# Optimization experiments

Measured on AMD Instinct MI355X. Metric: run time of the kernel, lower is better.

Reference implementation:

```python
import jax, jax.numpy as jnp
import numpy as np

D_MODEL = 1024
NUM_HEADS = 16
HEAD_DIM = D_MODEL // NUM_HEADS
B, S = 4, 2048


def setup_inputs() -> dict:
    key = jax.random.key(0)
    ks = jax.random.split(key, 11)
    scale = 1.0 / np.sqrt(D_MODEL)
    return {
        "query": jax.random.normal(ks[0], (B, S, D_MODEL), dtype=jnp.float32),
        "key": jax.random.normal(ks[1], (B, S, D_MODEL), dtype=jnp.float32),
        "value": jax.random.normal(ks[2], (B, S, D_MODEL), dtype=jnp.float32),
        "Wq": jax.random.normal(ks[3], (D_MODEL, D_MODEL), dtype=jnp.float32) * scale,
        "bq": jnp.zeros((D_MODEL,), dtype=jnp.float32),
        "Wk": jax.random.normal(ks[4], (D_MODEL, D_MODEL), dtype=jnp.float32) * scale,
        "bk": jnp.zeros((D_MODEL,), dtype=jnp.float32),
        "Wv": jax.random.normal(ks[5], (D_MODEL, D_MODEL), dtype=jnp.float32) * scale,
        "bv": jnp.zeros((D_MODEL,), dtype=jnp.float32),
        "Wo": jax.random.normal(ks[6], (D_MODEL, D_MODEL), dtype=jnp.float32) * scale,
        "bo": jnp.zeros((D_MODEL,), dtype=jnp.float32),
    }


def reference(query, key, value, Wq, bq, Wk, bk, Wv, bv, Wo, bo):
    b = query.shape[0]
    # QKV projections, split into heads: [B, H, S, hd]
    Q = (query @ Wq + bq).reshape(b, -1, NUM_HEADS, HEAD_DIM).transpose(0, 2, 1, 3)
    K = (key @ Wk + bk).reshape(b, -1, NUM_HEADS, HEAD_DIM).transpose(0, 2, 1, 3)
    V = (value @ Wv + bv).reshape(b, -1, NUM_HEADS, HEAD_DIM).transpose(0, 2, 1, 3)
    # scaled dot-product attention, full [B, H, S, S] scores (as in original)
    scores = jnp.einsum("bhqd,bhkd->bhqk", Q, K) / jnp.sqrt(
        jnp.asarray(HEAD_DIM, dtype=jnp.float32))
    attn = jax.nn.softmax(scores, axis=-1)
    out = jnp.einsum("bhqk,bhkd->bhqd", attn, V)
    out = out.transpose(0, 2, 1, 3).reshape(b, -1, D_MODEL)
    return out @ Wo + bo
```

## Files before the change

### kernel.cpp

```cpp
#include <hip/hip_runtime.h>
#include <hip/hip_bf16.h>

typedef _Float16 f16;
typedef _Float16 f16x8 __attribute__((ext_vector_type(8)));
typedef _Float16 f16x4 __attribute__((ext_vector_type(4)));
typedef __fp16 h16x2 __attribute__((ext_vector_type(2)));
typedef float f32x4 __attribute__((ext_vector_type(4)));

#define D_MODEL 1024
#define NHEAD 16
#define HD 64
#define BATCH 4
#define SEQ 2048
#define TOK (BATCH * SEQ)

__device__ __forceinline__ void gload_lds16(const void* g, void* l) {
  __builtin_amdgcn_global_load_lds(
      (const __attribute__((address_space(1))) unsigned int*)g,
      (__attribute__((address_space(3))) unsigned int*)l, 16, 0, 0);
}

__device__ __forceinline__ f16x8 fragF16_64(const char* rowptr, int g, int c) {
  union { uint4 u; f16x8 v; } r;
  r.u = *reinterpret_cast<const uint4*>(rowptr + ((g * 16) ^ ((c & 3) << 4)));
  return r.v;
}
__device__ __forceinline__ f16x8 fragF32_128(const char* rowptr, int g, int c) {
  const int s = (c & 7) << 4;
  union { uint4 u; float f[4]; } a, b;
  a.u = *reinterpret_cast<const uint4*>(rowptr + ((g * 32) ^ s));
  b.u = *reinterpret_cast<const uint4*>(rowptr + ((g * 32 + 16) ^ s));
  f16x8 r;
  r[0] = (f16)a.f[0]; r[1] = (f16)a.f[1]; r[2] = (f16)a.f[2]; r[3] = (f16)a.f[3];
  r[4] = (f16)b.f[0]; r[5] = (f16)b.f[1]; r[6] = (f16)b.f[2]; r[7] = (f16)b.f[3];
  return r;
}
__device__ __forceinline__ f16x8 lds_frag(const char* rowptr, int cb0, int s) {
  const uint2 a = *reinterpret_cast<const uint2*>(rowptr + (cb0 ^ s));
  const uint2 b = *reinterpret_cast<const uint2*>(rowptr + ((cb0 + 32) ^ s));
  union { unsigned int u[4]; f16x8 v; } r;
  r.u[0] = a.x; r.u[1] = a.y; r.u[2] = b.x; r.u[3] = b.y;
  return r.v;
}

__global__ __launch_bounds__(256) void transpose_cvt4_k(
    const float* __restrict__ w0, const float* __restrict__ w1,
    const float* __restrict__ w2, const float* __restrict__ w3,
    f16* __restrict__ t0, f16* __restrict__ t1, f16* __restrict__ t2,
    f16* __restrict__ t3) {
  __shared__ float tile[32][33];
  const float* W = blockIdx.z == 0 ? w0 : blockIdx.z == 1 ? w1 : blockIdx.z == 2 ? w2 : w3;
  f16* Wt = blockIdx.z == 0 ? t0 : blockIdx.z == 1 ? t1 : blockIdx.z == 2 ? t2 : t3;
  int n0 = blockIdx.x * 32, k0 = blockIdx.y * 32;
  int tx = threadIdx.x & 31, ty = threadIdx.x >> 5;
#pragma unroll
  for (int i = 0; i < 32; i += 8)
    tile[ty + i][tx] = W[(size_t)(k0 + ty + i) * D_MODEL + n0 + tx];
  __syncthreads();
#pragma unroll
  for (int i = 0; i < 32; i += 8)
    Wt[(size_t)(n0 + ty + i) * D_MODEL + k0 + tx] = (f16)tile[tx][ty + i];
}

__device__ __forceinline__ void swz_map(int& btx, int& bty) {
  int lin = blockIdx.x + blockIdx.y * 8;
  int xcd = lin & 7, rest = lin >> 3;
  bty = xcd * 8 + (rest & 7);
  btx = rest >> 3;
}

template <bool A_F32, bool B_F32, bool OUT_F32, bool BIAS_ROW>
__device__ __forceinline__ void gemm_body(
    const void* __restrict__ Ap, const void* __restrict__ Bp,
    const float* __restrict__ bias, void* __restrict__ Cout,
    int M, int N, int K, float scale, int btx, int bty) {
  constexpr int ABUF = A_F32 ? 16384 : 8192;
  constexpr int BBUF = B_F32 ? 16384 : 8192;
  constexpr int BUF = ABUF + BBUF;
  constexpr int NA = A_F32 ? 4 : 2;
  constexpr int NB = B_F32 ? 4 : 2;
  __shared__ char smem[2 * BUF];
  const int tid = threadIdx.x;
  const int lane = tid & 63, wid = tid >> 6;
  const int g = lane >> 4, c = lane & 15;
  const int wm = wid >> 1, wn = wid & 1;
  const size_t brow = (size_t)bty * 128, bcol = (size_t)btx * 128;

  f32x4 acc[4][4];
#pragma unroll
  for (int i = 0; i < 4; ++i)
#pragma unroll
    for (int j = 0; j < 4; ++j) acc[i][j] = (f32x4){0.f, 0.f, 0.f, 0.f};

  const char* ga[NA];
  const char* gb[NB];
#pragma unroll
  for (int j = 0; j < NA; ++j) {
    int ch = wid * NA + j;
    if constexpr (A_F32) {
      int row = ch * 8 + (lane >> 3);
      ga[j] = (const char*)Ap + ((size_t)(brow + row) * K) * 4 +
              (((lane & 7) * 16) ^ ((row & 7) << 4));
    } else {
      int row = ch * 16 + (lane >> 2);
      ga[j] = (const char*)Ap + ((size_t)(brow + row) * K) * 2 +
              (((lane & 3) * 16) ^ ((row & 3) << 4));
    }
  }
#pragma unroll
  for (int j = 0; j < NB; ++j) {
    int ch = wid * NB + j;
    if constexpr (B_F32) {
      int row = ch * 8 + (lane >> 3);
      gb[j] = (const char*)Bp + ((size_t)(bcol + row) * K) * 4 +
              (((lane & 7) * 16) ^ ((row & 7) << 4));
    } else {
      int row = ch * 16 + (lane >> 2);
      gb[j] = (const char*)Bp + ((size_t)(bcol + row) * K) * 2 +
              (((lane & 3) * 16) ^ ((row & 3) << 4));
    }
  }
  auto stage = [&](char* buf) {
#pragma unroll
    for (int j = 0; j < NA; ++j) {
      gload_lds16(ga[j], buf + (wid * NA + j) * 1024);
      ga[j] += A_F32 ? 128 : 64;
    }
#pragma unroll
    for (int j = 0; j < NB; ++j) {
      gload_lds16(gb[j], buf + ABUF + (wid * NB + j) * 1024);
      gb[j] += B_F32 ? 128 : 64;
    }
  };

  stage(smem);
  const int nt = K / 32;
  for (int t = 0; t < nt; ++t) {
    char* cur = smem + (size_t)(t & 1) * BUF;
    char* nxt = smem + (size_t)((t + 1) & 1) * BUF;
    asm volatile("s_waitcnt vmcnt(0)" ::: "memory");
    __syncthreads();
    if (t + 1 < nt) stage(nxt);

    f16x8 Af[4], Bf[4];
#pragma unroll
    for (int fm = 0; fm < 4; ++fm) {
      int row = wm * 64 + fm * 16 + c;
      if constexpr (A_F32) Af[fm] = fragF32_128(cur + row * 128, g, c);
      else Af[fm] = fragF16_64(cur + row * 64, g, c);
    }
#pragma unroll
    for (int fn = 0; fn < 4; ++fn) {
      int row = wn * 64 + fn * 16 + c;
      if constexpr (B_F32) Bf[fn] = fragF32_128(cur + ABUF + row * 128, g, c);
      else Bf[fn] = fragF16_64(cur + ABUF + row * 64, g, c);
    }
#pragma unroll
    for (int fm = 0; fm < 4; ++fm)
#pragma unroll
      for (int fn = 0; fn < 4; ++fn)
        acc[fm][fn] = __builtin_amdgcn_mfma_f32_16x16x32_f16(Af[fm], Bf[fn],
                                                             acc[fm][fn], 0, 0, 0);
  }

#pragma unroll
  for (int fn = 0; fn < 4; ++fn) {
    size_t col = bcol + wn * 64 + fn * 16 + c;
    float cbias = BIAS_ROW ? 0.f : bias[col];
#pragma unroll
    for (int fm = 0; fm < 4; ++fm) {
#pragma unroll
      for (int r = 0; r < 4; ++r) {
        size_t row = brow + wm * 64 + fm * 16 + g * 4 + r;
        float v = (acc[fm][fn][r] + (BIAS_ROW ? bias[row] : cbias)) * scale;
        if (OUT_F32)
          ((float*)Cout)[row * (size_t)N + col] = v;
        else
          ((f16*)Cout)[row * (size_t)N + col] = (f16)v;
      }
    }
  }
}

template <bool A_F32, bool B_F32, bool OUT_F32, bool BIAS_ROW, bool SWZ>
__global__ __launch_bounds__(256) void gemm_k(
    const void* __restrict__ Ap, const void* __restrict__ Bp,
    const float* __restrict__ bias, void* __restrict__ Cout,
    int M, int N, int K, float scale) {
  int btx, bty;
  if constexpr (SWZ) swz_map(btx, bty);
  else { btx = blockIdx.x; bty = blockIdx.y; }
  gemm_body<A_F32, B_F32, OUT_F32, BIAS_ROW>(Ap, Bp, bias, Cout, M, N, K, scale,
                                             btx, bty);
}

__global__ __launch_bounds__(256) void qkproj_k(
    const float* __restrict__ q32, const float* __restrict__ k32,
    const f16* __restrict__ Wqt, const f16* __restrict__ Wkt,
    const float* __restrict__ bq, const float* __restrict__ bk,
    f16* __restrict__ Qp, f16* __restrict__ Kp, float qscale) {
  int btx, bty;
  swz_map(btx, bty);
  const void* Ap = blockIdx.z ? (const void*)k32 : (const void*)q32;
  const void* Bp = blockIdx.z ? (const void*)Wkt : (const void*)Wqt;
  const float* bias = blockIdx.z ? bk : bq;
  void* Cout = blockIdx.z ? (void*)Kp : (void*)Qp;
  float scale = blockIdx.z ? 1.0f : qscale;
  gemm_body<true, false, false, false>(Ap, Bp, bias, Cout, TOK, D_MODEL,
                                       D_MODEL, scale, btx, bty);
}

__global__ __launch_bounds__(512) void attn_k(const f16* __restrict__ Q,
                                              const f16* __restrict__ Kp,
                                              const f16* __restrict__ Vt,
                                              f16* __restrict__ AO) {
  __shared__ char smem[65536];
  const int tid = threadIdx.x, lane = tid & 63, wid = tid >> 6;
  const int g = lane >> 4, c = lane & 15;
  const int b = blockIdx.x >> 4, h = blockIdx.x & 15;
  const int qt = blockIdx.y;
  const size_t qrow0 = (size_t)b * SEQ + (size_t)qt * 256;
  const int sr = lane >> 3;
  const int sc = (lane & 7) * 16;
  const float NEG_M = -8.65617025f;
  constexpr int NT = SEQ / 64;

#pragma unroll
  for (int j = 0; j < 4; ++j) {
    int ch = wid * 4 + j;
    int row = ch * 8 + sr;
    const char* gq = (const char*)Q + ((qrow0 + row) * D_MODEL + h * HD) * 2 +
                     (sc ^ (sr << 4));
    gload_lds16(gq, smem + ch * 1024);
  }
  asm volatile("s_waitcnt vmcnt(0)" ::: "memory");
  __syncthreads();

  f16x8 Qf[2][2];
#pragma unroll
  for (int fq = 0; fq < 2; ++fq) {
    int row = wid * 32 + fq * 16 + c;
#pragma unroll
    for (int kk = 0; kk < 2; ++kk) {
      union { uint4 u; f16x8 v; } r;
      r.u = *reinterpret_cast<const uint4*>(
          smem + row * 128 + ((kk * 64 + g * 16) ^ ((c & 7) << 4)));
      Qf[fq][kk] = r.v;
    }
  }
  __syncthreads();

  const char* gk;
  const char* gv;
  {
    int row = wid * 8 + sr;
    gk = (const char*)Kp + (((size_t)b * SEQ + row) * D_MODEL + h * HD) * 2 +
         (sc ^ (sr << 4));
    gv = (const char*)Vt + ((size_t)(h * HD + row) * TOK + (size_t)b * SEQ) * 2 +
         (sc ^ (sr << 4));
  }
#pragma unroll
  for (int tt = 0; tt < 3; ++tt) {
    gload_lds16(gk, smem + tt * 8192 + wid * 1024);
    gload_lds16(gv, smem + 32768 + tt * 8192 + wid * 1024);
    gk += (size_t)64 * D_MODEL * 2;
    gv += 64 * 2;
  }

  f16x8 ones_f;
#pragma unroll
  for (int j = 0; j < 8; ++j) ones_f[j] = (c == 0) ? (f16)1.0f : (f16)0.0f;

  f32x4 o[4][2];
#pragma unroll
  for (int i = 0; i < 4; ++i)
#pragma unroll
    for (int j = 0; j < 2; ++j) o[i][j] = (f32x4){0.f, 0.f, 0.f, 0.f};
  f32x4 o_l[2] = {(f32x4){0.f, 0.f, 0.f, 0.f}, (f32x4){0.f, 0.f, 0.f, 0.f}};

  for (int t = 0; t < NT; ++t) {
    if (t < NT - 2)
      asm volatile("s_waitcnt vmcnt(4)" ::: "memory");
    else if (t == NT - 2)
      asm volatile("s_waitcnt vmcnt(2)" ::: "memory");
    else
      asm volatile("s_waitcnt vmcnt(0)" ::: "memory");
    __builtin_amdgcn_s_barrier();
    asm volatile("" ::: "memory");
    if (t + 3 < NT) {
      gload_lds16(gk, smem + ((t + 3) & 3) * 8192 + wid * 1024);
      gload_lds16(gv, smem + 32768 + ((t + 3) & 3) * 8192 + wid * 1024);
      gk += (size_t)64 * D_MODEL * 2;
      gv += 64 * 2;
    }
    const char* Ks = smem + (t & 3) * 8192;
    const char* Vs = smem + 32768 + (t & 3) * 8192;

    f32x4 st[4][2];
#pragma unroll
    for (int i = 0; i < 4; ++i)
#pragma unroll
      for (int j = 0; j < 2; ++j)
        st[i][j] = (f32x4){NEG_M, NEG_M, NEG_M, NEG_M};
#pragma unroll
    for (int kk = 0; kk < 2; ++kk) {
      f16x8 Kf[4];
#pragma unroll
      for (int km = 0; km < 4; ++km) {
        int row = km * 16 + c;
        union { uint4 u; f16x8 v; } r;
        r.u = *reinterpret_cast<const uint4*>(
            Ks + row * 128 + ((kk * 64 + g * 16) ^ ((c & 7) << 4)));
        Kf[km] = r.v;
      }
      __builtin_amdgcn_s_setprio(1);
#pragma unroll
      for (int km = 0; km < 4; ++km)
#pragma unroll
        for (int fq = 0; fq < 2; ++fq)
          st[km][fq] = __builtin_amdgcn_mfma_f32_16x16x32_f16(Kf[km], Qf[fq][kk],
                                                              st[km][fq], 0, 0, 0);
      __builtin_amdgcn_s_setprio(0);
    }

    f16x8 pb[2][2];
#pragma unroll
    for (int fq = 0; fq < 2; ++fq) {
#pragma unroll
      for (int km = 0; km < 4; ++km)
#pragma unroll
        for (int r = 0; r < 4; ++r)
          st[km][fq][r] = __builtin_amdgcn_exp2f(st[km][fq][r]);
#pragma unroll
      for (int k2 = 0; k2 < 2; ++k2) {
        union { h16x2 h2[4]; f16x8 v; } u;
        u.h2[0] = __builtin_amdgcn_cvt_pkrtz(st[2 * k2][fq][0], st[2 * k2][fq][1]);
        u.h2[1] = __builtin_amdgcn_cvt_pkrtz(st[2 * k2][fq][2], st[2 * k2][fq][3]);
        u.h2[2] = __builtin_amdgcn_cvt_pkrtz(st[2 * k2 + 1][fq][0], st[2 * k2 + 1][fq][1]);
        u.h2[3] = __builtin_amdgcn_cvt_pkrtz(st[2 * k2 + 1][fq][2], st[2 * k2 + 1][fq][3]);
        pb[k2][fq] = u.v;
      }
    }

#pragma unroll
    for (int k2 = 0; k2 < 2; ++k2) {
      f16x8 Vf[4];
#pragma unroll
      for (int fhd = 0; fhd < 4; ++fhd) {
        int row = fhd * 16 + c;
        Vf[fhd] = lds_frag(Vs + row * 128, k2 * 64 + g * 8, (row & 7) << 4);
      }
      __builtin_amdgcn_s_setprio(1);
#pragma unroll
      for (int fhd = 0; fhd < 4; ++fhd)
#pragma unroll
        for (int fq = 0; fq < 2; ++fq)
          o[fhd][fq] = __builtin_amdgcn_mfma_f32_16x16x32_f16(Vf[fhd], pb[k2][fq],
                                                              o[fhd][fq], 0, 0, 0);
#pragma unroll
      for (int fq = 0; fq < 2; ++fq)
        o_l[fq] = __builtin_amdgcn_mfma_f32_16x16x32_f16(ones_f, pb[k2][fq],
                                                         o_l[fq], 0, 0, 0);
      __builtin_amdgcn_s_setprio(0);
    }
  }

#pragma unroll
  for (int fq = 0; fq < 2; ++fq) {
    float L = __shfl(o_l[fq][0], c);
    float rl = 1.0f / L;
    size_t token = qrow0 + wid * 32 + fq * 16 + c;
#pragma unroll
    for (int fhd = 0; fhd < 4; ++fhd) {
      f16x4 vv;
#pragma unroll
      for (int r = 0; r < 4; ++r) vv[r] = (f16)(o[fhd][fq][r] * rl);
      *reinterpret_cast<f16x4*>(AO + token * D_MODEL + h * HD + fhd * 16 + g * 4) = vv;
    }
  }
}

extern "C" void kernel_launch(void* const* d_in, const int* in_sizes, int n_in,
                              void* d_out, int out_size, void* d_ws, size_t ws_size,
                              hipStream_t stream) {
  const float* q32 = (const float*)d_in[0];
  const float* k32 = (const float*)d_in[1];
  const float* v32 = (const float*)d_in[2];
  const float* Wq = (const float*)d_in[3];
  const float* bq = (const float*)d_in[4];
  const float* Wk = (const float*)d_in[5];
  const float* bk = (const float*)d_in[6];
  const float* Wv = (const float*)d_in[7];
  const float* bv = (const float*)d_in[8];
  const float* Wo = (const float*)d_in[9];
  const float* bo = (const float*)d_in[10];

  const size_t TOKD = (size_t)TOK * D_MODEL;
  const size_t WD = (size_t)D_MODEL * D_MODEL;
  f16* Qp = (f16*)d_ws;
  f16* Kp = Qp + TOKD;
  f16* Vt = Kp + TOKD;
  f16* AO = Vt + TOKD;
  f16* Wqt = AO + TOKD;
  f16* Wkt = Wqt + WD;
  f16* Wvt = Wkt + WD;
  f16* Wot = Wvt + WD;

  dim3 tg(32, 32, 4);
  transpose_cvt4_k<<<tg, 256, 0, stream>>>(Wq, Wk, Wv, Wo, Wqt, Wkt, Wvt, Wot);

  dim3 gqk(8, 64, 2);
  qkproj_k<<<gqk, 256, 0, stream>>>(q32, k32, Wqt, Wkt, bq, bk, Qp, Kp,
                                    0.18033688f);
  dim3 gv(TOK / 128, D_MODEL / 128);
  gemm_k<false, true, false, true, false><<<gv, 256, 0, stream>>>(
      Wvt, v32, bv, Vt, D_MODEL, TOK, D_MODEL, 1.0f);

  dim3 ga(BATCH * NHEAD, SEQ / 256);
  attn_k<<<ga, 512, 0, stream>>>(Qp, Kp, Vt, AO);

  dim3 gq(D_MODEL / 128, TOK / 128);
  gemm_k<false, false, true, false, true><<<gq, 256, 0, stream>>>(
      AO, Wot, bo, (float*)d_out, TOK, D_MODEL, D_MODEL, 1.0f);
}
```

Baseline: 194.4 us.

## Inline QK projection GEMM with 128x256 tiles and custom XCD block mapping

Replaces the generic gemm_body call in the Q/K projection kernel with an inlined GEMM that uses 128x256 output tiles, so each wave computes 64x128 with 4x8 MFMA fragments. This cuts the grid from 8x64 to 4x64 per projection, and a new block-to-tile mapping groups row tiles per XCD. The aim is more reuse per loaded A/B tile and better L2 locality. The trade-off is higher register pressure from 32 accumulators and fewer blocks for occupancy. The output stores are also scattered 2-byte writes.

```diff
diff --git a/kernel.cpp b/kernel.cpp
--- a/kernel.cpp
+++ b/kernel.cpp
@@ -199,15 +199,102 @@
     const f16* __restrict__ Wqt, const f16* __restrict__ Wkt,
     const float* __restrict__ bq, const float* __restrict__ bk,
     f16* __restrict__ Qp, f16* __restrict__ Kp, float qscale) {
-  int btx, bty;
-  swz_map(btx, bty);
-  const void* Ap = blockIdx.z ? (const void*)k32 : (const void*)q32;
-  const void* Bp = blockIdx.z ? (const void*)Wkt : (const void*)Wqt;
+  int lin = blockIdx.x + blockIdx.y * 4;
+  int xcd = lin & 7, rest = lin >> 3;
+  int bty = xcd * 8 + (rest & 7);
+  int btx = rest >> 3;
+  const float* Ap = blockIdx.z ? k32 : q32;
+  const f16* Bp = blockIdx.z ? Wkt : Wqt;
   const float* bias = blockIdx.z ? bk : bq;
-  void* Cout = blockIdx.z ? (void*)Kp : (void*)Qp;
-  float scale = blockIdx.z ? 1.0f : qscale;
-  gemm_body<true, false, false, false>(Ap, Bp, bias, Cout, TOK, D_MODEL,
-                                       D_MODEL, scale, btx, bty);
+  f16* Cout = blockIdx.z ? Kp : Qp;
+  const float scale = blockIdx.z ? 1.0f : qscale;
+  const int K = D_MODEL;
+
+  __shared__ char smem[65536];
+  const int tid = threadIdx.x;
+  const int lane = tid & 63, wid = tid >> 6;
+  const int g = lane >> 4, c = lane & 15;
+  const int wm = wid >> 1, wn = wid & 1;
+  const size_t brow = (size_t)bty * 128, bcol = (size_t)btx * 256;
+
+  f32x4 acc[4][8];
+#pragma unroll
+  for (int i = 0; i < 4; ++i)
+#pragma unroll
+    for (int j = 0; j < 8; ++j) acc[i][j] = (f32x4){0.f, 0.f, 0.f, 0.f};
+
+  const char* ga[4];
+  const char* gb[4];
+#pragma unroll
+  for (int j = 0; j < 4; ++j) {
+    int ch = wid * 4 + j;
+    int row = ch * 8 + (lane >> 3);
+    ga[j] = (const char*)Ap + ((size_t)(brow + row) * K) * 4 +
+            (((lane & 7) * 16) ^ ((row & 7) << 4));
+  }
+#pragma unroll
+  for (int j = 0; j < 4; ++j) {
+    int ch = wid * 4 + j;
+    int row = ch * 16 + (lane >> 2);
+    gb[j] = (const char*)Bp + ((size_t)(bcol + row) * K) * 2 +
+            (((lane & 3) * 16) ^ ((row & 3) << 4));
+  }
+  auto stage = [&](char* buf) {
+#pragma unroll
+    for (int j = 0; j < 4; ++j) {
+      gload_lds16(ga[j], buf + (wid * 4 + j) * 1024);
+      ga[j] += 128;
+    }
+#pragma unroll
+    for (int j = 0; j < 4; ++j) {
+      gload_lds16(gb[j], buf + 16384 + (wid * 4 + j) * 1024);
+      gb[j] += 64;
+    }
+  };
+
+  stage(smem);
+  const int nt = K / 32;
+  for (int t = 0; t < nt; ++t) {
+    char* cur = smem + (size_t)(t & 1) * 32768;
+    char* nxt = smem + (size_t)((t + 1) & 1) * 32768;
+    asm volatile("s_waitcnt vmcnt(0)" ::: "memory");
+    __syncthreads();
+    if (t + 1 < nt) stage(nxt);
+
+    f16x8 Af[4], Bf[8];
+#pragma unroll
+    for (int fm = 0; fm < 4; ++fm) {
+      int row = wm * 64 + fm * 16 + c;
+      Af[fm] = fragF32_128(cur + row * 128, g, c);
+    }
+#pragma unroll
+    for (int fn = 0; fn < 8; ++fn) {
+      int row = wn * 128 + fn * 16 + c;
+      Bf[fn] = fragF16_64(cur + 16384 + row * 64, g, c);
+    }
+    __builtin_amdgcn_s_setprio(1);
+#pragma unroll
+    for (int fm = 0; fm < 4; ++fm)
+#pragma unroll
+      for (int fn = 0; fn < 8; ++fn)
+        acc[fm][fn] = __builtin_amdgcn_mfma_f32_16x16x32_f16(Af[fm], Bf[fn],
+                                                             acc[fm][fn], 0, 0, 0);
+    __builtin_amdgcn_s_setprio(0);
+  }
+
+#pragma unroll
+  for (int fn = 0; fn < 8; ++fn) {
+    size_t col = bcol + wn * 128 + fn * 16 + c;
+    float cbias = bias[col];
+#pragma unroll
+    for (int fm = 0; fm < 4; ++fm) {
+#pragma unroll
+      for (int r = 0; r < 4; ++r) {
+        size_t row = brow + wm * 64 + fm * 16 + g * 4 + r;
+        Cout[row * (size_t)D_MODEL + col] = (f16)((acc[fm][fn][r] + cbias) * scale);
+      }
+    }
+  }
 }
 
 __global__ __launch_bounds__(512) void attn_k(const f16* __restrict__ Q,
@@ -409,7 +496,7 @@
   dim3 tg(32, 32, 4);
   transpose_cvt4_k<<<tg, 256, 0, stream>>>(Wq, Wk, Wv, Wo, Wqt, Wkt, Wvt, Wot);
 
-  dim3 gqk(8, 64, 2);
+  dim3 gqk(D_MODEL / 256, TOK / 128, 2);
   qkproj_k<<<gqk, 256, 0, stream>>>(q32, k32, Wqt, Wkt, bq, bk, Qp, Kp,
                                     0.18033688f);
   dim3 gv(TOK / 128, D_MODEL / 128);
```

New measurement: 192.5 us. No clear change (-1.0%).
